# Optimization experiments

Measured on AMD Instinct MI355X. Metric: run time of the kernel, lower is better.

The kernel has to match this reference:

```python
import jax, jax.numpy as jnp
import numpy as np

N = 50000      # nodes
E = 800000     # edges (before self-loops)
FEAT = 128     # input feature dim F
HID = 32       # per-head hidden H
HEADS = 8      # n_head
C = 40         # classes
NEG_SLOPE = 0.2


def setup_inputs() -> dict:
    key = jax.random.key(0)
    ks = jax.random.split(key, 12)
    x = jax.random.normal(ks[0], (N, FEAT), jnp.float32)
    edge_index = jax.random.randint(ks[1], (2, E), 0, N, jnp.int32)
    s1 = 1.0 / np.sqrt(FEAT)
    s2 = 1.0 / np.sqrt(HEADS * HID)
    W1 = jax.random.normal(ks[2], (FEAT, HEADS * HID), jnp.float32) * s1
    a1_src = jax.random.normal(ks[3], (HEADS, HID), jnp.float32) * s2
    a1_dst = jax.random.normal(ks[4], (HEADS, HID), jnp.float32) * s2
    b1 = jnp.zeros((HEADS * HID,), jnp.float32)
    W2 = jax.random.normal(ks[5], (HEADS * HID, HEADS * HID), jnp.float32) * s2
    a2_src = jax.random.normal(ks[6], (HEADS, HID), jnp.float32) * s2
    a2_dst = jax.random.normal(ks[7], (HEADS, HID), jnp.float32) * s2
    b2 = jnp.zeros((HEADS * HID,), jnp.float32)
    Wc = jax.random.normal(ks[8], (HEADS * HID, C), jnp.float32) * s2
    bc = jnp.zeros((C,), jnp.float32)
    return {"x": x, "edge_index": edge_index,
            "W1": W1, "a1_src": a1_src, "a1_dst": a1_dst, "b1": b1,
            "W2": W2, "a2_src": a2_src, "a2_dst": a2_dst, "b2": b2,
            "Wc": Wc, "bc": bc}


def gat_conv(x, src, dst, W, a_src, a_dst, b):
    # x: [N, F_in] -> per-head features [N, heads, H]
    n = x.shape[0]
    xh = (x @ W).reshape(n, HEADS, HID)
    alpha_s = jnp.einsum('nhd,hd->nh', xh, a_src)   # [N, heads]
    alpha_d = jnp.einsum('nhd,hd->nh', xh, a_dst)   # [N, heads]
    e = alpha_s[src] + alpha_d[dst]                  # [E, heads]
    e = jnp.where(e > 0, e, NEG_SLOPE * e)           # LeakyReLU(0.2)
    # softmax over incoming edges grouped by destination node
    emax = jax.ops.segment_max(e, dst, num_segments=n)
    ex = jnp.exp(e - emax[dst])
    denom = jax.ops.segment_sum(ex, dst, num_segments=n)
    alpha = ex / denom[dst]                          # [E, heads]
    msg = xh[src] * alpha[:, :, None]                # [E, heads, H]
    out = jax.ops.segment_sum(msg, dst, num_segments=n)
    return out.reshape(n, HEADS * HID) + b


def reference(x, edge_index, W1, a1_src, a1_dst, b1, W2, a2_src, a2_dst, b2, Wc, bc):
    # PyG GATConv adds self-loops by default
    loops = jnp.arange(N, dtype=edge_index.dtype)
    ei = jnp.concatenate([edge_index, jnp.stack([loops, loops])], axis=1)
    src, dst = ei[0], ei[1]
    h = gat_conv(x, src, dst, W1, a1_src, a1_dst, b1)
    h = jax.nn.relu(h)
    h = gat_conv(h, src, dst, W2, a2_src, a2_dst, b2)
    h = jax.nn.relu(h)
    return h @ Wc + bc
```

## Files before the change

### kernel.cpp

```cpp
#include <hip/hip_runtime.h>
#include <math.h>

#define NNODES 50000
#define NEDGES 800000
#define NTOT   850000
#define NHEAD  8
#define HDIM   32
#define HHD    256
#define NCLS   40
#define NEG_SLOPE 0.2f

typedef _Float16 half4 __attribute__((ext_vector_type(4)));
typedef _Float16 half8 __attribute__((ext_vector_type(8)));
typedef float f32x16 __attribute__((ext_vector_type(16)));
typedef unsigned short u16;


__global__ void k_init_counts(int* __restrict__ counts) {
    int i = blockIdx.x * 256 + threadIdx.x;
    if (i < NNODES) counts[i] = 1;
}

__global__ void k_count(const int* __restrict__ ei, int* __restrict__ counts) {
    int i = blockIdx.x * 256 + threadIdx.x;
    if (i < NEDGES) atomicAdd(&counts[ei[NEDGES + i]], 1);
}

__global__ __launch_bounds__(256) void k_scan1(const int* __restrict__ counts,
                                               int* __restrict__ partial,
                                               int* __restrict__ bsums) {
    __shared__ int lds[256];
    int t = threadIdx.x;
    int i = blockIdx.x * 256 + t;
    int v = (i < NNODES) ? counts[i] : 0;
    lds[t] = v;
    __syncthreads();
    for (int off = 1; off < 256; off <<= 1) {
        int add = (t >= off) ? lds[t - off] : 0;
        __syncthreads();
        lds[t] += add;
        __syncthreads();
    }
    if (i < NNODES) partial[i] = lds[t] - v;
    if (t == 255) bsums[blockIdx.x] = lds[255];
}

__global__ __launch_bounds__(256) void k_scan2(const int* __restrict__ bsums,
                                               int* __restrict__ boff, int nb) {
    __shared__ int lds[256];
    int t = threadIdx.x;
    int v = (t < nb) ? bsums[t] : 0;
    lds[t] = v;
    __syncthreads();
    for (int off = 1; off < 256; off <<= 1) {
        int add = (t >= off) ? lds[t - off] : 0;
        __syncthreads();
        lds[t] += add;
        __syncthreads();
    }
    if (t < nb) boff[t] = lds[t] - v;
}

__global__ void k_scan3(int* __restrict__ row_ptr, const int* __restrict__ boff,
                        int* __restrict__ cursor) {
    int i = blockIdx.x * 256 + threadIdx.x;
    if (i < NNODES) {
        int r = row_ptr[i] + boff[blockIdx.x];
        row_ptr[i] = r;
        cursor[i] = r;
    }
    if (i == 0) row_ptr[NNODES] = NTOT;
}

__global__ void k_scatter(const int* __restrict__ ei, int* __restrict__ cursor,
                          int* __restrict__ esrc) {
    int i = blockIdx.x * 256 + threadIdx.x;
    if (i < NEDGES) {
        int s = ei[i];
        int d = ei[NEDGES + i];
        int pos = atomicAdd(&cursor[d], 1);
        esrc[pos] = s;
    } else if (i < NTOT) {
        int n = i - NEDGES;
        int pos = atomicAdd(&cursor[n], 1);
        esrc[pos] = n;
    }
}

__global__ void k_prep_all(const float* __restrict__ W1, const float* __restrict__ W2,
                           const float* __restrict__ Wc,
                           _Float16* __restrict__ w1t, _Float16* __restrict__ w2t,
                           _Float16* __restrict__ wct) {
    int gid = blockIdx.x * 256 + threadIdx.x;
    if (gid >= 256 * 64) return;
    int frag = gid >> 6, l = gid & 63;
    const float* W; _Float16* Wt; int K, Nc, fkn, fbase;
    if (frag < 64)       { W = W1; Wt = w1t; K = 128; Nc = 256; fkn = 8;  fbase = 0; }
    else if (frag < 192) { W = W2; Wt = w2t; K = 256; Nc = 256; fkn = 16; fbase = 64; }
    else                 { W = Wc; Wt = wct; K = 256; Nc = 40;  fkn = 16; fbase = 192; }
    int f = frag - fbase;
    int fn = f / fkn, fk = f - fn * fkn;
    int n = fn * 32 + (l & 31);
    int k = fk * 16 + ((l >> 5) << 3);
    half8 v;
    #pragma unroll
    for (int j = 0; j < 8; ++j)
        v[j] = (n < Nc) ? (_Float16)W[(size_t)(k + j) * Nc + n] : (_Float16)0.f;
    *reinterpret_cast<half8*>(Wt + ((size_t)f * 64 + l) * 8) = v;
}

#define TBM 128
#define TBN 128
#define TBK 32
#define APAD 34

template <typename AT, bool FUSE_ALPHA>
__global__ __launch_bounds__(256) void k_mfma_gemm(
    const AT* __restrict__ A,
    const _Float16* __restrict__ Wt,
    const float* __restrict__ bias,
    _Float16* __restrict__ Ch,
    float* __restrict__ Cf,
    const float* __restrict__ a_src,
    const float* __restrict__ a_dst,
    float* __restrict__ alpha_s,
    float* __restrict__ alpha_d,
    int M, int K, int NcReal, int ldc)
{
    constexpr bool A_IS_F32 = sizeof(AT) == 4;
    constexpr int CT_ROWS = FUSE_ALPHA ? TBM : 1;
    __shared__ _Float16 Ah[TBM][APAD];
    __shared__ _Float16 Ct[CT_ROWS][TBN + 4];
    int t = threadIdx.x;
    int lane = t & 63;
    int wid = t >> 6;
    int wr = wid >> 1, wc = wid & 1;
    int rowBase = blockIdx.y * TBM;
    int colBase = blockIdx.x * TBN;

    int arow = t >> 1;
    int akoff = (t & 1) * 16;
    bool arow_ok = (rowBase + arow) < M;
    const AT* aptr = A + (size_t)(rowBase + arow) * K + akoff;

    int fkn = K >> 4;
    size_t bbase[2];
    #pragma unroll
    for (int ct = 0; ct < 2; ++ct) {
        int fn = blockIdx.x * 4 + wc * 2 + ct;
        bbase[ct] = ((size_t)fn * fkn) * 512 + (size_t)lane * 8;
    }

    f32x16 acc[2][2];
    #pragma unroll
    for (int i = 0; i < 2; ++i)
        #pragma unroll
        for (int j = 0; j < 2; ++j)
            #pragma unroll
            for (int r = 0; r < 16; ++r) acc[i][j][r] = 0.f;

    float4 aregf[4];
    half8  aregh[2];
    auto load_a = [&](const AT* ap) {
        if constexpr (A_IS_F32) {
            #pragma unroll
            for (int i = 0; i < 4; ++i)
                aregf[i] = arow_ok ? *reinterpret_cast<const float4*>((const float*)ap + i * 4)
                                   : float4{0.f, 0.f, 0.f, 0.f};
        } else {
            #pragma unroll
            for (int i = 0; i < 2; ++i)
                aregh[i] = arow_ok ? *reinterpret_cast<const half8*>((const _Float16*)ap + i * 8)
                                   : half8{0, 0, 0, 0, 0, 0, 0, 0};
        }
    };
    load_a(aptr);

    for (int k0 = 0; k0 < K; k0 += TBK) {
        if constexpr (A_IS_F32) {
            half8 h0, h1;
            #pragma unroll
            for (int c = 0; c < 4; ++c) {
                float4 v = aregf[c];
                if (c < 2) {
                    h0[c * 4 + 0] = (_Float16)v.x; h0[c * 4 + 1] = (_Float16)v.y;
                    h0[c * 4 + 2] = (_Float16)v.z; h0[c * 4 + 3] = (_Float16)v.w;
                } else {
                    h1[(c - 2) * 4 + 0] = (_Float16)v.x; h1[(c - 2) * 4 + 1] = (_Float16)v.y;
                    h1[(c - 2) * 4 + 2] = (_Float16)v.z; h1[(c - 2) * 4 + 3] = (_Float16)v.w;
                }
            }
            *reinterpret_cast<half8*>(&Ah[arow][akoff])     = h0;
            *reinterpret_cast<half8*>(&Ah[arow][akoff + 8]) = h1;
        } else {
            *reinterpret_cast<half8*>(&Ah[arow][akoff])     = aregh[0];
            *reinterpret_cast<half8*>(&Ah[arow][akoff + 8]) = aregh[1];
        }
        __syncthreads();
        if (k0 + TBK < K) load_a(aptr + k0 + TBK);
        #pragma unroll
        for (int sub = 0; sub < 2; ++sub) {
            int kfo = sub * 16 + (lane >> 5) * 8;
            half8 ah[2];
            #pragma unroll
            for (int rt = 0; rt < 2; ++rt) {
                int r = wr * 64 + rt * 32 + (lane & 31);
                ah[rt] = *reinterpret_cast<const half8*>(&Ah[r][kfo]);
            }
            half8 bh[2];
            int fidx = (k0 >> 4) + sub;
            #pragma unroll
            for (int ct = 0; ct < 2; ++ct)
                bh[ct] = *reinterpret_cast<const half8*>(Wt + bbase[ct] + (size_t)fidx * 512);
            #pragma unroll
            for (int rt = 0; rt < 2; ++rt)
                #pragma unroll
                for (int ct = 0; ct < 2; ++ct)
                    acc[rt][ct] = __builtin_amdgcn_mfma_f32_32x32x16_f16(
                        ah[rt], bh[ct], acc[rt][ct], 0, 0, 0);
        }
        __syncthreads();
    }

    #pragma unroll
    for (int rt = 0; rt < 2; ++rt)
        #pragma unroll
        for (int ct = 0; ct < 2; ++ct) {
            int lcol = wc * 64 + ct * 32 + (lane & 31);
            int col = colBase + lcol;
            #pragma unroll
            for (int r = 0; r < 16; ++r) {
                int lrow = wr * 64 + rt * 32 + (r & 3) + 8 * (r >> 2) + 4 * (lane >> 5);
                int row = rowBase + lrow;
                float v = acc[rt][ct][r];
                _Float16 hv = (_Float16)v;
                if constexpr (FUSE_ALPHA) Ct[lrow][lcol] = hv;
                if (row >= M) continue;
                if (Ch) {
                    Ch[(size_t)row * ldc + col] = hv;
                } else if (col < NcReal) {
                    Cf[(size_t)row * ldc + col] = v + bias[col];
                }
            }
        }

    if constexpr (FUSE_ALPHA) {
        __syncthreads();
        #pragma unroll
        for (int idx = t; idx < TBM * 4; idx += 256) {
            int lrow = idx >> 2, hoff = idx & 3;
            int grow = rowBase + lrow;
            if (grow < M) {
                int h = blockIdx.x * 4 + hoff;
                const float* as4 = a_src + h * HDIM;
                const float* ad4 = a_dst + h * HDIM;
                float ss = 0.f, sd = 0.f;
                #pragma unroll
                for (int j = 0; j < HDIM; ++j) {
                    float v = (float)Ct[lrow][hoff * 32 + j];
                    ss += v * as4[j];
                    sd += v * ad4[j];
                }
                alpha_s[grow * NHEAD + h] = ss;
                alpha_d[grow * NHEAD + h] = sd;
            }
        }
    }
}

__global__ __launch_bounds__(256) void k_agg(const _Float16* __restrict__ xh,
                                             const float* __restrict__ alpha_s,
                                             const float* __restrict__ alpha_d,
                                             const int* __restrict__ row_ptr,
                                             const int* __restrict__ esrc,
                                             const float* __restrict__ bias,
                                             _Float16* __restrict__ out) {
    int wave = blockIdx.x * 4 + (threadIdx.x >> 6);
    int node = wave * 2 + ((threadIdx.x & 63) >> 5);
    if (node >= NNODES) return;
    int l = threadIdx.x & 31;
    int h = l >> 2;
    int beg = row_ptr[node], end = row_ptr[node + 1];
    float ad = alpha_d[node * NHEAD + h];
    float acc[8] = {};
    float ssum = 0.f;
    int i = beg;
    for (; i + 3 < end; i += 4) {
        int s0 = esrc[i], s1 = esrc[i + 1], s2 = esrc[i + 2], s3 = esrc[i + 3];
        float e0 = alpha_s[s0 * NHEAD + h] + ad;
        float e1 = alpha_s[s1 * NHEAD + h] + ad;
        float e2 = alpha_s[s2 * NHEAD + h] + ad;
        float e3 = alpha_s[s3 * NHEAD + h] + ad;
        half8 v0 = *reinterpret_cast<const half8*>(xh + (size_t)s0 * HHD + l * 8);
        half8 v1 = *reinterpret_cast<const half8*>(xh + (size_t)s1 * HHD + l * 8);
        half8 v2 = *reinterpret_cast<const half8*>(xh + (size_t)s2 * HHD + l * 8);
        half8 v3 = *reinterpret_cast<const half8*>(xh + (size_t)s3 * HHD + l * 8);
        e0 = (e0 > 0.f) ? e0 : NEG_SLOPE * e0;
        e1 = (e1 > 0.f) ? e1 : NEG_SLOPE * e1;
        e2 = (e2 > 0.f) ? e2 : NEG_SLOPE * e2;
        e3 = (e3 > 0.f) ? e3 : NEG_SLOPE * e3;
        float p0 = __expf(e0), p1 = __expf(e1), p2 = __expf(e2), p3 = __expf(e3);
        ssum += (p0 + p1) + (p2 + p3);
        #pragma unroll
        for (int d = 0; d < 8; ++d)
            acc[d] += p0 * (float)v0[d] + p1 * (float)v1[d] +
                      p2 * (float)v2[d] + p3 * (float)v3[d];
    }
    for (; i < end; ++i) {
        int s0 = esrc[i];
        float e0 = alpha_s[s0 * NHEAD + h] + ad;
        half8 v0 = *reinterpret_cast<const half8*>(xh + (size_t)s0 * HHD + l * 8);
        e0 = (e0 > 0.f) ? e0 : NEG_SLOPE * e0;
        float p0 = __expf(e0);
        ssum += p0;
        #pragma unroll
        for (int d = 0; d < 8; ++d)
            acc[d] += p0 * (float)v0[d];
    }
    float inv = 1.f / ssum;
    float4 b0 = *reinterpret_cast<const float4*>(bias + l * 8);
    float4 b1 = *reinterpret_cast<const float4*>(bias + l * 8 + 4);
    float bb[8] = {b0.x, b0.y, b0.z, b0.w, b1.x, b1.y, b1.z, b1.w};
    half8 r;
    #pragma unroll
    for (int d = 0; d < 8; ++d)
        r[d] = (_Float16)fmaxf(acc[d] * inv + bb[d], 0.f);
    *reinterpret_cast<half8*>(out + (size_t)node * HHD + l * 8) = r;
}


extern "C" void kernel_launch(void* const* d_in, const int* in_sizes, int n_in,
                              void* d_out, int out_size, void* d_ws, size_t ws_size,
                              hipStream_t stream) {
    const float* x   = (const float*)d_in[0];
    const int*   ei  = (const int*)  d_in[1];
    const float* W1  = (const float*)d_in[2];
    const float* a1s = (const float*)d_in[3];
    const float* a1d = (const float*)d_in[4];
    const float* b1  = (const float*)d_in[5];
    const float* W2  = (const float*)d_in[6];
    const float* a2s = (const float*)d_in[7];
    const float* a2d = (const float*)d_in[8];
    const float* b2  = (const float*)d_in[9];
    const float* Wc  = (const float*)d_in[10];
    const float* bc  = (const float*)d_in[11];
    float* out = (float*)d_out;

    char* ws = (char*)d_ws;
    size_t off = 0;
    auto alloc = [&](size_t bytes) -> void* {
        void* p = ws + off;
        off += (bytes + 255) & ~(size_t)255;
        return p;
    };
    _Float16* xh_h   = (_Float16*)alloc((size_t)NNODES * HHD * 2);
    _Float16* hbuf_h = (_Float16*)alloc((size_t)NNODES * HHD * 2);
    float* as_   = (float*)alloc((size_t)NNODES * NHEAD * 4);
    float* ad_   = (float*)alloc((size_t)NNODES * NHEAD * 4);
    int* counts  = (int*)alloc((size_t)NNODES * 4);
    int* row_ptr = (int*)alloc((size_t)(NNODES + 1) * 4);
    int* cursor  = (int*)alloc((size_t)NNODES * 4);
    int* esrc    = (int*)alloc((size_t)NTOT * 4);
    int* bsums   = (int*)alloc(256 * 4);
    int* boff    = (int*)alloc(256 * 4);
    _Float16* w1t = (_Float16*)alloc((size_t)64 * 64 * 8 * 2);
    _Float16* w2t = (_Float16*)alloc((size_t)128 * 64 * 8 * 2);
    _Float16* wct = (_Float16*)alloc((size_t)64 * 64 * 8 * 2);
    (void)ws_size; (void)in_sizes; (void)n_in; (void)out_size;

    int gn = (NNODES + 255) / 256;
    int ge = (NEDGES + 255) / 256;
    int gt = (NTOT + 255) / 256;

    k_init_counts<<<gn, 256, 0, stream>>>(counts);
    k_count<<<ge, 256, 0, stream>>>(ei, counts);
    k_scan1<<<gn, 256, 0, stream>>>(counts, row_ptr, bsums);
    k_scan2<<<1, 256, 0, stream>>>(bsums, boff, gn);
    k_scan3<<<gn, 256, 0, stream>>>(row_ptr, boff, cursor);
    k_scatter<<<gt, 256, 0, stream>>>(ei, cursor, esrc);

    k_prep_all<<<64, 256, 0, stream>>>(W1, W2, Wc, w1t, w2t, wct);

    dim3 gHid(HHD / TBN, (NNODES + TBM - 1) / TBM);
    dim3 gCls(1, (NNODES + TBM - 1) / TBM);
    int gagg = NNODES / 8;

    k_mfma_gemm<float, true><<<gHid, 256, 0, stream>>>(
        x, w1t, nullptr, xh_h, nullptr, a1s, a1d, as_, ad_, NNODES, 128, HHD, HHD);
    k_agg<<<gagg, 256, 0, stream>>>(xh_h, as_, ad_, row_ptr, esrc, b1, hbuf_h);

    k_mfma_gemm<_Float16, true><<<gHid, 256, 0, stream>>>(
        hbuf_h, w2t, nullptr, xh_h, nullptr, a2s, a2d, as_, ad_, NNODES, HHD, HHD, HHD);
    k_agg<<<gagg, 256, 0, stream>>>(xh_h, as_, ad_, row_ptr, esrc, b2, hbuf_h);

    k_mfma_gemm<_Float16, false><<<gCls, 256, 0, stream>>>(
        hbuf_h, wct, bc, nullptr, out, nullptr, nullptr, nullptr, nullptr,
        NNODES, HHD, NCLS, NCLS);
}
```

Measured before the change: 336.4 us.

## Fuse classifier GEMM into layer-2 aggregation and compute alpha via wave shuffles

The final classifier GEMM is folded into the second aggregation kernel. Each half-wave dot-products its ReLU'd 256-wide row against a transposed fp16 Wc and reduces across lanes with xor shuffles, which removes one kernel launch and the write and re-read of the hidden buffer. The GEMM epilogue now computes the attention logits directly from the accumulator registers with butterfly shuffles, dropping the shared-memory C tile and its extra barrier. The cost is 40 classes × 5 shuffle steps per node in the aggregation tail, more register pressure from the 40-entry partial array, and many redundant shuffles in the alpha reduction.

```diff
diff --git a/kernel.cpp b/kernel.cpp
--- a/kernel.cpp
+++ b/kernel.cpp
@@ -90,23 +90,29 @@
 __global__ void k_prep_all(const float* __restrict__ W1, const float* __restrict__ W2,
                            const float* __restrict__ Wc,
                            _Float16* __restrict__ w1t, _Float16* __restrict__ w2t,
-                           _Float16* __restrict__ wct) {
+                           _Float16* __restrict__ wcT) {
     int gid = blockIdx.x * 256 + threadIdx.x;
-    if (gid >= 256 * 64) return;
-    int frag = gid >> 6, l = gid & 63;
-    const float* W; _Float16* Wt; int K, Nc, fkn, fbase;
-    if (frag < 64)       { W = W1; Wt = w1t; K = 128; Nc = 256; fkn = 8;  fbase = 0; }
-    else if (frag < 192) { W = W2; Wt = w2t; K = 256; Nc = 256; fkn = 16; fbase = 64; }
-    else                 { W = Wc; Wt = wct; K = 256; Nc = 40;  fkn = 16; fbase = 192; }
-    int f = frag - fbase;
-    int fn = f / fkn, fk = f - fn * fkn;
-    int n = fn * 32 + (l & 31);
-    int k = fk * 16 + ((l >> 5) << 3);
-    half8 v;
-    #pragma unroll
-    for (int j = 0; j < 8; ++j)
-        v[j] = (n < Nc) ? (_Float16)W[(size_t)(k + j) * Nc + n] : (_Float16)0.f;
-    *reinterpret_cast<half8*>(Wt + ((size_t)f * 64 + l) * 8) = v;
+    if (gid < 192 * 64) {
+        int frag = gid >> 6, l = gid & 63;
+        const float* W; _Float16* Wt; int K, fkn, fbase;
+        if (frag < 64) { W = W1; Wt = w1t; K = 128; fkn = 8;  fbase = 0; }
+        else           { W = W2; Wt = w2t; K = 256; fkn = 16; fbase = 64; }
+        int f = frag - fbase;
+        int fn = f / fkn, fk = f - fn * fkn;
+        int n = fn * 32 + (l & 31);
+        int k = fk * 16 + ((l >> 5) << 3);
+        half8 v;
+        #pragma unroll
+        for (int j = 0; j < 8; ++j)
+            v[j] = (_Float16)W[(size_t)(k + j) * HHD + n];
+        *reinterpret_cast<half8*>(Wt + ((size_t)f * 64 + l) * 8) = v;
+    } else {
+        int idx = gid - 192 * 64;
+        if (idx < NCLS * HHD) {
+            int c = idx >> 8, k = idx & 255;
+            wcT[idx] = (_Float16)Wc[(size_t)k * NCLS + c];
+        }
+    }
 }
 
 #define TBM 128
@@ -114,23 +120,19 @@
 #define TBK 32
 #define APAD 34
 
-template <typename AT, bool FUSE_ALPHA>
+template <typename AT>
 __global__ __launch_bounds__(256) void k_mfma_gemm(
     const AT* __restrict__ A,
     const _Float16* __restrict__ Wt,
-    const float* __restrict__ bias,
     _Float16* __restrict__ Ch,
-    float* __restrict__ Cf,
     const float* __restrict__ a_src,
     const float* __restrict__ a_dst,
     float* __restrict__ alpha_s,
     float* __restrict__ alpha_d,
-    int M, int K, int NcReal, int ldc)
+    int M, int K, int ldc)
 {
     constexpr bool A_IS_F32 = sizeof(AT) == 4;
-    constexpr int CT_ROWS = FUSE_ALPHA ? TBM : 1;
     __shared__ _Float16 Ah[TBM][APAD];
-    __shared__ _Float16 Ct[CT_ROWS][TBN + 4];
     int t = threadIdx.x;
     int lane = t & 63;
     int wid = t >> 6;
@@ -226,55 +228,55 @@
     for (int rt = 0; rt < 2; ++rt)
         #pragma unroll
         for (int ct = 0; ct < 2; ++ct) {
-            int lcol = wc * 64 + ct * 32 + (lane & 31);
-            int col = colBase + lcol;
+            int col = colBase + wc * 64 + ct * 32 + (lane & 31);
             #pragma unroll
             for (int r = 0; r < 16; ++r) {
-                int lrow = wr * 64 + rt * 32 + (r & 3) + 8 * (r >> 2) + 4 * (lane >> 5);
-                int row = rowBase + lrow;
+                int row = rowBase + wr * 64 + rt * 32 +
+                          (r & 3) + 8 * (r >> 2) + 4 * (lane >> 5);
+                if (row < M)
+                    Ch[(size_t)row * ldc + col] = (_Float16)acc[rt][ct][r];
+            }
+        }
+
+    #pragma unroll
+    for (int ct = 0; ct < 2; ++ct) {
+        int h = blockIdx.x * 4 + wc * 2 + ct;
+        float asv = a_src[h * HDIM + (lane & 31)];
+        float adv = a_dst[h * HDIM + (lane & 31)];
+        #pragma unroll
+        for (int rt = 0; rt < 2; ++rt) {
+            #pragma unroll
+            for (int r = 0; r < 16; ++r) {
                 float v = acc[rt][ct][r];
-                _Float16 hv = (_Float16)v;
-                if constexpr (FUSE_ALPHA) Ct[lrow][lcol] = hv;
-                if (row >= M) continue;
-                if (Ch) {
-                    Ch[(size_t)row * ldc + col] = hv;
-                } else if (col < NcReal) {
-                    Cf[(size_t)row * ldc + col] = v + bias[col];
+                float ps = v * asv;
+                float pd = v * adv;
+                #pragma unroll
+                for (int m = 1; m <= 16; m <<= 1) {
+                    ps += __shfl_xor(ps, m, 64);
+                    pd += __shfl_xor(pd, m, 64);
+                }
+                int row = rowBase + wr * 64 + rt * 32 +
+                          (r & 3) + 8 * (r >> 2) + 4 * (lane >> 5);
+                if ((lane & 31) == r && row < M) {
+                    alpha_s[row * NHEAD + h] = ps;
+                    alpha_d[row * NHEAD + h] = pd;
                 }
             }
         }
-
-    if constexpr (FUSE_ALPHA) {
-        __syncthreads();
-        #pragma unroll
-        for (int idx = t; idx < TBM * 4; idx += 256) {
-            int lrow = idx >> 2, hoff = idx & 3;
-            int grow = rowBase + lrow;
-            if (grow < M) {
-                int h = blockIdx.x * 4 + hoff;
-                const float* as4 = a_src + h * HDIM;
-                const float* ad4 = a_dst + h * HDIM;
-                float ss = 0.f, sd = 0.f;
-                #pragma unroll
-                for (int j = 0; j < HDIM; ++j) {
-                    float v = (float)Ct[lrow][hoff * 32 + j];
-                    ss += v * as4[j];
-                    sd += v * ad4[j];
-                }
-                alpha_s[grow * NHEAD + h] = ss;
-                alpha_d[grow * NHEAD + h] = sd;
-            }
-        }
-    }
-}
-
+    }
+}
+
+template <bool FUSE_CLS>
 __global__ __launch_bounds__(256) void k_agg(const _Float16* __restrict__ xh,
                                              const float* __restrict__ alpha_s,
                                              const float* __restrict__ alpha_d,
                                              const int* __restrict__ row_ptr,
                                              const int* __restrict__ esrc,
                                              const float* __restrict__ bias,
-                                             _Float16* __restrict__ out) {
+                                             _Float16* __restrict__ out_h,
+                                             const _Float16* __restrict__ WcT,
+                                             const float* __restrict__ bc,
+                                             float* __restrict__ out_f) {
     int wave = blockIdx.x * 4 + (threadIdx.x >> 6);
     int node = wave * 2 + ((threadIdx.x & 63) >> 5);
     if (node >= NNODES) return;
@@ -321,11 +323,39 @@
     float4 b0 = *reinterpret_cast<const float4*>(bias + l * 8);
     float4 b1 = *reinterpret_cast<const float4*>(bias + l * 8 + 4);
     float bb[8] = {b0.x, b0.y, b0.z, b0.w, b1.x, b1.y, b1.z, b1.w};
-    half8 r;
+    float rl[8];
     #pragma unroll
     for (int d = 0; d < 8; ++d)
-        r[d] = (_Float16)fmaxf(acc[d] * inv + bb[d], 0.f);
-    *reinterpret_cast<half8*>(out + (size_t)node * HHD + l * 8) = r;
+        rl[d] = fmaxf(acc[d] * inv + bb[d], 0.f);
+
+    if constexpr (!FUSE_CLS) {
+        half8 r;
+        #pragma unroll
+        for (int d = 0; d < 8; ++d) r[d] = (_Float16)rl[d];
+        *reinterpret_cast<half8*>(out_h + (size_t)node * HHD + l * 8) = r;
+    } else {
+        float part[NCLS];
+        #pragma unroll
+        for (int c = 0; c < NCLS; ++c) {
+            half8 w = *reinterpret_cast<const half8*>(WcT + (size_t)c * HHD + l * 8);
+            float s = 0.f;
+            #pragma unroll
+            for (int d = 0; d < 8; ++d) s += rl[d] * (float)w[d];
+            part[c] = s;
+        }
+        #pragma unroll
+        for (int c = 0; c < NCLS; ++c) {
+            #pragma unroll
+            for (int m = 1; m <= 16; m <<= 1)
+                part[c] += __shfl_xor(part[c], m, 64);
+        }
+        if (l == 0) {
+            float* op = out_f + (size_t)node * NCLS;
+            #pragma unroll
+            for (int c = 0; c < NCLS; ++c)
+                op[c] = part[c] + bc[c];
+        }
+    }
 }
 
 
@@ -365,7 +395,7 @@
     int* boff    = (int*)alloc(256 * 4);
     _Float16* w1t = (_Float16*)alloc((size_t)64 * 64 * 8 * 2);
     _Float16* w2t = (_Float16*)alloc((size_t)128 * 64 * 8 * 2);
-    _Float16* wct = (_Float16*)alloc((size_t)64 * 64 * 8 * 2);
+    _Float16* wcT = (_Float16*)alloc((size_t)NCLS * HHD * 2);
     (void)ws_size; (void)in_sizes; (void)n_in; (void)out_size;
 
     int gn = (NNODES + 255) / 256;
@@ -379,21 +409,19 @@
     k_scan3<<<gn, 256, 0, stream>>>(row_ptr, boff, cursor);
     k_scatter<<<gt, 256, 0, stream>>>(ei, cursor, esrc);
 
-    k_prep_all<<<64, 256, 0, stream>>>(W1, W2, Wc, w1t, w2t, wct);
+    k_prep_all<<<(192 * 64 + NCLS * HHD + 255) / 256, 256, 0, stream>>>(
+        W1, W2, Wc, w1t, w2t, wcT);
 
     dim3 gHid(HHD / TBN, (NNODES + TBM - 1) / TBM);
-    dim3 gCls(1, (NNODES + TBM - 1) / TBM);
     int gagg = NNODES / 8;
 
-    k_mfma_gemm<float, true><<<gHid, 256, 0, stream>>>(
-        x, w1t, nullptr, xh_h, nullptr, a1s, a1d, as_, ad_, NNODES, 128, HHD, HHD);
-    k_agg<<<gagg, 256, 0, stream>>>(xh_h, as_, ad_, row_ptr, esrc, b1, hbuf_h);
-
-    k_mfma_gemm<_Float16, true><<<gHid, 256, 0, stream>>>(
-        hbuf_h, w2t, nullptr, xh_h, nullptr, a2s, a2d, as_, ad_, NNODES, HHD, HHD, HHD);
-    k_agg<<<gagg, 256, 0, stream>>>(xh_h, as_, ad_, row_ptr, esrc, b2, hbuf_h);
-
-    k_mfma_gemm<_Float16, false><<<gCls, 256, 0, stream>>>(
-        hbuf_h, wct, bc, nullptr, out, nullptr, nullptr, nullptr, nullptr,
-        NNODES, HHD, NCLS, NCLS);
-}
+    k_mfma_gemm<float><<<gHid, 256, 0, stream>>>(
+        x, w1t, xh_h, a1s, a1d, as_, ad_, NNODES, 128, HHD);
+    k_agg<false><<<gagg, 256, 0, stream>>>(xh_h, as_, ad_, row_ptr, esrc, b1,
+                                           hbuf_h, nullptr, nullptr, nullptr);
+
+    k_mfma_gemm<_Float16><<<gHid, 256, 0, stream>>>(
+        hbuf_h, w2t, xh_h, a2s, a2d, as_, ad_, NNODES, HHD, HHD);
+    k_agg<true><<<gagg, 256, 0, stream>>>(xh_h, as_, ad_, row_ptr, esrc, b2,
+                                          nullptr, wcT, bc, out);
+}
```

Result: slower. 415.4 us (+23.5%).
